# Kernel tuning notes

Measured on AMD Instinct MI355X. Metric: run time of the kernel, lower is better.

Reference implementation:

```python
import jax, jax.numpy as jnp
import numpy as np
from jax import lax

B, IN_C, DIM, HEADS, K = 8, 64, 128, 4, 3
H, W = 96, 96
HEAD_DIM = DIM // HEADS
SCALE = HEAD_DIM ** -0.5
EPS = 1e-5  # BatchNorm eps (eval mode, running_mean=0, running_var=1)


def _conv3x3(x, w):
    return lax.conv_general_dilated(x, w, (1, 1), ((1, 1), (1, 1)),
                                    dimension_numbers=('NCHW', 'OIHW', 'NCHW'))


def _cbr(x, w, g, b):
    y = _conv3x3(x, w)
    y = y * (g / jnp.sqrt(1.0 + EPS))[None, :, None, None] + b[None, :, None, None]
    return jax.nn.relu(y)


def setup_inputs() -> dict:
    key = jax.random.key(0)
    ks = jax.random.split(key, 24)
    n = lambda i, s, sc=0.05: jax.random.normal(ks[i], s, jnp.float32) * sc
    u = lambda i, s: jax.random.uniform(ks[i], s, jnp.float32, 0.5, 1.5)
    return dict(
        x=jax.random.normal(ks[0], (B, IN_C, H, W), jnp.float32),
        fg=jax.random.normal(ks[1], (B, DIM, H, W), jnp.float32),
        conv1_w=n(2, (DIM, IN_C, 3, 3)), bn1_g=u(3, (DIM,)), bn1_b=n(4, (DIM,)),
        conv2_w=n(5, (DIM, DIM, 3, 3)), bn2_g=u(6, (DIM,)), bn2_b=n(7, (DIM,)),
        v_w=n(8, (DIM, DIM)), v_b=n(9, (DIM,)),
        attn_w=n(10, (K ** 4 * HEADS, DIM)), attn_b=n(11, (K ** 4 * HEADS,)),
        proj_w=n(12, (DIM, DIM)), proj_b=n(13, (DIM,)),
        conv3_w=n(14, (DIM, DIM, 3, 3)), bn3_g=u(15, (DIM,)), bn3_b=n(16, (DIM,)),
        conv4_w=n(17, (DIM, DIM, 3, 3)), bn4_g=u(18, (DIM,)), bn4_b=n(19, (DIM,)),
    )


def reference(x, fg, conv1_w, bn1_g, bn1_b, conv2_w, bn2_g, bn2_b,
              v_w, v_b, attn_w, attn_b, proj_w, proj_b,
              conv3_w, bn3_g, bn3_b, conv4_w, bn4_g, bn4_b):
    L = H * W
    # input_cbr: two conv3x3 + BN(eval) + ReLU
    xf = _cbr(_cbr(x, conv1_w, bn1_g, bn1_b), conv2_w, bn2_g, bn2_b)  # (B,DIM,H,W)
    xh = xf.transpose(0, 2, 3, 1)                 # (B,H,W,DIM)
    fgh = fg.transpose(0, 2, 3, 1)                # (B,H,W,DIM)
    # value projection then unfold (im2col, channel-major patch ordering like torch)
    v = (xh @ v_w.T + v_b).transpose(0, 3, 1, 2)  # (B,DIM,H,W)
    patches = lax.conv_general_dilated_patches(v, (K, K), (1, 1), ((1, 1), (1, 1)))  # (B,DIM*9,H,W)
    vp = patches.reshape(B, HEADS, HEAD_DIM, K * K, L).transpose(0, 1, 4, 3, 2)  # (B,h,L,9,hd)
    # attention logits directly from fg (stride=1 -> AvgPool identity)
    attn = (fgh @ attn_w.T + attn_b).reshape(B, L, HEADS, K * K, K * K)
    attn = attn.transpose(0, 2, 1, 3, 4) * SCALE  # (B,h,L,9,9)
    attn = jax.nn.softmax(attn, axis=-1)
    # batched small matmuls: (9,9) @ (9,hd) per window
    xw = jnp.einsum('bhlpq,bhlqd->bhlpd', attn, vp)  # (B,h,L,9,hd)
    xw = xw.transpose(0, 1, 4, 3, 2).reshape(B, DIM, K, K, H, W)  # channel-major, then (kh,kw)
    # fold: overlapping scatter-add back to (H,W)
    canvas = jnp.zeros((B, DIM, H + 2, W + 2), xw.dtype)
    for ki in range(K):
        for kj in range(K):
            canvas = canvas.at[:, :, ki:ki + H, kj:kj + W].add(xw[:, :, ki, kj])
    folded = canvas[:, :, 1:H + 1, 1:W + 1]        # crop padding
    p = (folded.transpose(0, 2, 3, 1) @ proj_w.T + proj_b).transpose(0, 3, 1, 2)
    # output_cbr
    out = _cbr(_cbr(p, conv3_w, bn3_g, bn3_b), conv4_w, bn4_g, bn4_b)
    return out
```

## Files before the change

### kernel.cpp

```cpp
#include <hip/hip_runtime.h>
#include <math.h>

typedef __attribute__((ext_vector_type(8))) short short8;
typedef __attribute__((ext_vector_type(4))) float f32x4;
typedef unsigned short u16;
typedef unsigned int u32;

#define HW   96
#define LPIX 9216
static constexpr float kScale = 0.17677669529663687f;

__device__ inline u16 f2bf(float f) {
    u32 x = __float_as_uint(f);
    return (u16)((x + 0x7fffu + ((x >> 16) & 1u)) >> 16);
}
__device__ inline float bf2f(u16 v) { return __uint_as_float((u32)v << 16); }

typedef __attribute__((address_space(1))) const void gas_t;
typedef __attribute__((address_space(3))) void las_t;
__device__ __forceinline__ void g2lds16(const void* g, void* l) {
    __builtin_amdgcn_global_load_lds((gas_t*)g, (las_t*)l, 16, 0, 0);
}

#define WAITV(n) do {                                                   \
        asm volatile("s_waitcnt vmcnt(" #n ")" ::: "memory");           \
        __builtin_amdgcn_sched_barrier(0);                              \
    } while (0)
#define SFENCE() __builtin_amdgcn_sched_barrier(0)

__global__ __launch_bounds__(256) void cast_nchw_nhwc_all(
    const float* __restrict__ x, const float* __restrict__ fg,
    u16* __restrict__ xb, u16* __restrict__ fgb)
{
    const int y = blockIdx.x, b = blockIdx.y, tid = threadIdx.x;
    const int isfg = blockIdx.z;
    const float* in = isfg ? fg : x;
    u16* out = isfg ? fgb : xb;
    const int C = isfg ? 128 : 64;

    __shared__ float sT[HW * 128];
    for (int i = tid; i < HW * C; i += 256) {
        int c = i / HW, xx = i - c * HW;
        sT[xx * C + c] = in[(((size_t)b * C + c) * HW + y) * HW + xx];
    }
    __syncthreads();
    for (int i = tid; i < HW * (C / 8); i += 256) {
        int c8 = i % (C / 8), xx = i / (C / 8);
        union { short8 v8; u16 u[8]; } pk;
#pragma unroll
        for (int j = 0; j < 8; ++j) pk.u[j] = f2bf(sT[xx * C + c8 * 8 + j]);
        *(short8*)&out[(((size_t)b * HW + y) * HW + xx) * C + c8 * 8] = pk.v8;
    }
}

__device__ __forceinline__ void conv_w_decode(
    int i, int CIN, int& co, int& ci, int& f)
{
    int e  = i & 7;
    int gr = i >> 3;
    int c  = gr / 4608;
    int gi = gr - c * 4608;
    f  = gi >> 9;
    int rr = gi & 511;
    int ch = rr >> 8;
    int m  = (rr >> 2) & 63;
    int s  = rr & 3;
    int qq = (s - (m >> 1)) & 3;
    co = ch * 64 + m;
    ci = c * 32 + qq * 8 + e;
    (void)CIN;
}

__device__ __forceinline__ void conv_w_elem(
    const float* __restrict__ w, u16* __restrict__ wp, int CIN, int i)
{
    int co, ci, f;
    conv_w_decode(i, CIN, co, ci, f);
    wp[i] = f2bf(w[(size_t)(co * CIN + ci) * 9 + f]);
}

__device__ __forceinline__ void attn_w_elem(
    const float* __restrict__ aw, u16* __restrict__ wp, int i)
{
    int e = i & 7;
    int g = i >> 3;
    int h = g / 1536, r = g - h * 1536;
    int c4 = r / 384, r2 = r - c4 * 384;
    int rr = r2 >> 2, s = r2 & 3;
    int qq = (s - (rr >> 1)) & 3;
    int ci = c4 * 32 + qq * 8 + e;
    float v = (rr < 81) ? aw[(size_t)(h * 81 + rr) * 128 + ci] : 0.f;
    wp[i] = f2bf(v);
}

__global__ __launch_bounds__(256) void cast_weights_all(
    const float* __restrict__ c1w, const float* __restrict__ c2w,
    const float* __restrict__ c4w, const float* __restrict__ vw,
    const float* __restrict__ aw,
    u16* __restrict__ w1p, u16* __restrict__ w2p, u16* __restrict__ w4p,
    u16* __restrict__ vwp, u16* __restrict__ awp)
{
    int i = blockIdx.x * 256 + threadIdx.x;
    if (i < 73728)  { conv_w_elem(c1w, w1p, 64, i);  return; }
    i -= 73728;
    if (i < 147456) { conv_w_elem(c2w, w2p, 128, i); return; }
    i -= 147456;
    if (i < 147456) { conv_w_elem(c4w, w4p, 128, i); return; }
    i -= 147456;
    if (i < 16384)  { vwp[i] = f2bf(vw[i]); return; }
    i -= 16384;
    if (i < 49152)  attn_w_elem(aw, awp, i);
}

__global__ __launch_bounds__(128) void fuse_w3(
    const float* __restrict__ c3w, const float* __restrict__ pw,
    const float* __restrict__ pb,
    u16* __restrict__ w3p, float* __restrict__ bt)
{
    const int co = blockIdx.x;
    const int t  = threadIdx.x;
    __shared__ float sW[128 * 9];
    __shared__ float sB[9];

    {
        const float* src = &c3w[(size_t)co * 128 * 9];
        for (int i = t; i < 1152; i += 128) sW[i] = src[i];
    }
    __syncthreads();

    float acc[9];
#pragma unroll
    for (int f = 0; f < 9; ++f) acc[f] = 0.f;
#pragma unroll 4
    for (int ci = 0; ci < 128; ++ci) {
        float p = pw[ci * 128 + t];
#pragma unroll
        for (int f = 0; f < 9; ++f) acc[f] = fmaf(sW[ci * 9 + f], p, acc[f]);
    }
    {
        int m = co & 63, chh = co >> 6;
        int e = t & 7, qq = (t >> 3) & 3, c = t >> 5;
        int s = (qq + (m >> 1)) & 3;
#pragma unroll
        for (int f = 0; f < 9; ++f) {
            size_t gr = (size_t)c * 4608 + f * 512 + chh * 256 + m * 4 + s;
            w3p[gr * 8 + e] = f2bf(acc[f]);
        }
    }
    if (t < 9) {
        float a = 0.f;
        for (int ci = 0; ci < 128; ++ci) a = fmaf(sW[ci * 9 + t], pb[ci], a);
        sB[t] = a;
    }
    __syncthreads();
    if (t < 9) {
        float v;
        switch (t) {
            case 0: v = sB[0]+sB[1]+sB[2]+sB[3]+sB[4]+sB[5]+sB[6]+sB[7]+sB[8]; break;
            case 1: v = sB[0]+sB[1]+sB[2]; break;
            case 2: v = sB[6]+sB[7]+sB[8]; break;
            case 3: v = sB[0]+sB[3]+sB[6]; break;
            case 4: v = sB[2]+sB[5]+sB[8]; break;
            case 5: v = sB[0]; break;
            case 6: v = sB[2]; break;
            case 7: v = sB[6]; break;
            default: v = sB[8]; break;
        }
        bt[t * 128 + co] = v;
    }
}

template <int CIN, bool OUT_F32, bool PBC>
__global__ __launch_bounds__(768, 1) void conv_gemm(
    const u16* __restrict__ in, const u16* __restrict__ wp,
    const float* __restrict__ g, const float* __restrict__ be,
    const float* __restrict__ bt, void* outv)
{
    constexpr int NC   = CIN / 32;
    constexpr int WBYT = 73728;
    constexpr int HBYT = 36864;

    const int bx = blockIdx.x;
    const int b  = blockIdx.y;
    const int y0 = bx * 3;
    const int l0 = y0 * 96;

    const int tid = threadIdx.x, lane = tid & 63, wv = tid >> 6;
    const int half = wv & 1, ch = (wv >> 1) & 1, r = wv >> 2;
    const int lx = lane & 15, q = lane >> 4;

    __shared__ __align__(16) char smem[WBYT + 2 * HBYT];
    float* sT = (float*)smem;
    float* sF = (float*)smem;

    const int aoff = lx * 64 + (((q + (lx >> 1)) & 3) << 4);
    const int pb   = r * 96 + half * 48 + lx;

    f32x4 acc[4][3];
#pragma unroll
    for (int mt = 0; mt < 4; ++mt)
#pragma unroll
        for (int nt = 0; nt < 3; ++nt) acc[mt][nt] = (f32x4){0.f, 0.f, 0.f, 0.f};

    const u16* inb = in + (size_t)b * LPIX * CIN;

    auto STAGE_W = [&](int c) {
#pragma unroll
        for (int j = 0; j < 6; ++j) {
            g2lds16(&wp[((size_t)c * 4608 + j * 768 + tid) * 8],
                    (char*)smem + (j * 768 + wv * 64) * 16);
        }
    };
    auto STAGE_H = [&](int c, int buf) {
#pragma unroll
        for (int i = 0; i < 3; ++i) {
            int gi = i * 768 + tid;
            int p  = gi >> 2, s = gi & 3;
            int qq = (s - (p >> 1)) & 3;
            int lh = l0 - 96 + p;
            lh = lh < 0 ? 0 : (lh >= LPIX ? LPIX - 1 : lh);
            g2lds16(&inb[(size_t)lh * CIN + c * 32 + qq * 8],
                    (char*)smem + WBYT + buf * HBYT + (i * 768 + wv * 64) * 16);
        }
    };
    auto TAP = [&](int f, int hbuf) {
        const int dy = f / 3 - 1, dx = f % 3 - 1;
        const int off = dy * 96 + dx + 96;
        const bool vy = (unsigned)(y0 + r + dy) < 96u;
        const char* hb = (const char*)smem + WBYT + hbuf * HBYT;
        short8 af[4], bfr[3];
#pragma unroll
        for (int mt = 0; mt < 4; ++mt)
            af[mt] = *(const short8*)((const char*)smem + (f * 2 + ch) * 4096
                                      + mt * 1024 + aoff);
#pragma unroll
        for (int nt = 0; nt < 3; ++nt) {
            int pm = pb + nt * 16 + off;
            int slot = (q + (pm >> 1)) & 3;
            short8 t8 = *(const short8*)(hb + pm * 64 + slot * 16);
            bool ok = vy & ((unsigned)(half * 48 + nt * 16 + lx + dx) < 96u);
            bfr[nt] = ok ? t8 : (short8){0, 0, 0, 0, 0, 0, 0, 0};
        }
#pragma unroll
        for (int mt = 0; mt < 4; ++mt)
#pragma unroll
            for (int nt = 0; nt < 3; ++nt)
                acc[mt][nt] = __builtin_amdgcn_mfma_f32_16x16x32_bf16(
                    af[mt], bfr[nt], acc[mt][nt], 0, 0, 0);
    };

    STAGE_H(0, 0);
    SFENCE();
    STAGE_W(0);
    SFENCE();
    STAGE_H(1, 1);
    SFENCE();
    WAITV(3);
    __builtin_amdgcn_s_barrier();
    asm volatile("" ::: "memory");

#pragma unroll
    for (int c = 0; c < NC; ++c) {
        const int hbuf = c & 1;
        TAP(0, hbuf); TAP(1, hbuf); TAP(2, hbuf);
        TAP(3, hbuf); TAP(4, hbuf); TAP(5, hbuf);
        TAP(6, hbuf); TAP(7, hbuf); TAP(8, hbuf);
        if (c + 1 < NC) {
            asm volatile("s_waitcnt lgkmcnt(0)" ::: "memory");
            __builtin_amdgcn_s_barrier();
            asm volatile("" ::: "memory");
            STAGE_W(c + 1);
            SFENCE();
            if (c + 2 < NC) STAGE_H(c + 2, c & 1);
            SFENCE();
            if (c + 2 < NC) { WAITV(3); } else { WAITV(0); }
            __builtin_amdgcn_s_barrier();
            asm volatile("" ::: "memory");
        }
    }

    asm volatile("s_waitcnt lgkmcnt(0) vmcnt(0)" ::: "memory");
    __builtin_amdgcn_s_barrier();
    asm volatile("" ::: "memory");

    const float rs = rsqrtf(1.f + 1e-5f);
    if (OUT_F32) {
        float* out = (float*)outv;
#pragma unroll
        for (int hh = 0; hh < 2; ++hh) {
            if (hh) { __syncthreads(); }
            if (half == hh) {
#pragma unroll
                for (int mt = 0; mt < 4; ++mt)
#pragma unroll
                    for (int nt = 0; nt < 3; ++nt)
#pragma unroll
                        for (int reg = 0; reg < 4; ++reg)
                            sF[(ch * 64 + mt * 16 + q * 4 + reg) * 148
                               + r * 48 + nt * 16 + lx] = acc[mt][nt][reg];
            }
            __syncthreads();
            for (int i = tid; i < 4608; i += 768) {
                int co = i / 36, r2 = i - co * 36;
                int wrr = r2 / 12, j = r2 - wrr * 12;
                float sc = g[co] * rs, bb = be[co];
                f32x4 vv = *(const f32x4*)&sF[co * 148 + wrr * 48 + j * 4];
#pragma unroll
                for (int e = 0; e < 4; ++e) vv[e] = fmaxf(fmaf(vv[e], sc, bb), 0.f);
                *(f32x4*)&out[((size_t)b * 128 + co) * LPIX
                              + (y0 + wrr) * 96 + hh * 48 + j * 4] = vv;
            }
            if (!hh) __syncthreads();
        }
    } else {
        u16* out = (u16*)outv;
#pragma unroll
        for (int hh = 0; hh < 2; ++hh) {
            if (hh) { __syncthreads(); }
            if (half == hh) {
#pragma unroll
                for (int mt = 0; mt < 4; ++mt)
#pragma unroll
                    for (int nt = 0; nt < 3; ++nt)
#pragma unroll
                        for (int reg = 0; reg < 4; ++reg)
                            sT[(r * 48 + nt * 16 + lx) * 130
                               + ch * 64 + mt * 16 + q * 4 + reg] = acc[mt][nt][reg];
            }
            __syncthreads();
            for (int i = tid; i < 2304; i += 768) {
                int cog = i & 15, pxl = i >> 4;
                int wrr = pxl / 48, ofs = pxl - wrr * 48;
                int yy = y0 + wrr, xc = hh * 48 + ofs;
                int l = yy * 96 + xc;
                bool top = false, bot = false, lft = false, rgt = false;
                if (PBC) {
                    top = (yy == 0); bot = (yy == 95);
                    lft = (xc == 0); rgt = (xc == 95);
                }
                union { short8 v8; u16 u[8]; } pk;
#pragma unroll
                for (int j = 0; j < 8; ++j) {
                    int co = cog * 8 + j;
                    float val = sT[pxl * 130 + cog * 8 + j];
                    if (PBC) {
                        float corr = bt[co];
                        if (top) corr -= bt[128 + co];
                        if (bot) corr -= bt[256 + co];
                        if (lft) corr -= bt[384 + co];
                        if (rgt) corr -= bt[512 + co];
                        if (top && lft) corr += bt[640 + co];
                        if (top && rgt) corr += bt[768 + co];
                        if (bot && lft) corr += bt[896 + co];
                        if (bot && rgt) corr += bt[1024 + co];
                        val += corr;
                    }
                    pk.u[j] = f2bf(fmaxf(fmaf(val, g[co] * rs, be[co]), 0.f));
                }
                *(short8*)&out[((size_t)b * LPIX + l) * 128 + cog * 8] = pk.v8;
            }
            if (!hh) __syncthreads();
        }
    }
}

__global__ __launch_bounds__(256) void linear_mfma(
    const u16* __restrict__ in, const u16* __restrict__ wp,
    const float* __restrict__ bias, u16* __restrict__ out)
{
    const int l0 = blockIdx.x * 64;
    const int tid = threadIdx.x, lane = tid & 63, wv = tid >> 6;
    const int wm = wv >> 1, wn = wv & 1;
    const int lx = lane & 15, q = lane >> 4;

    __shared__ char smem[4 * 64 * 40 * 2 + 4 * 128 * 40 * 2];
    u16* sX = (u16*)smem;
    u16* sW = (u16*)(smem + 4 * 64 * 40 * 2);
    float* sT = (float*)smem;

    for (int i = tid; i < 1024; i += 256) {
        int k8 = i & 15, px = i >> 4;
        short8 v = *(const short8*)&in[((size_t)(l0 + px)) * 128 + k8 * 8];
        *(short8*)&sX[((k8 >> 2) * 64 + px) * 40 + (k8 & 3) * 8] = v;
    }
    for (int i = tid; i < 2048; i += 256) {
        int k8 = i & 15, co = i >> 4;
        short8 v = *(const short8*)&wp[(size_t)co * 128 + k8 * 8];
        *(short8*)&sW[((k8 >> 2) * 128 + co) * 40 + (k8 & 3) * 8] = v;
    }
    __syncthreads();

    f32x4 acc[4][2];
#pragma unroll
    for (int mt = 0; mt < 4; ++mt)
#pragma unroll
        for (int nt = 0; nt < 2; ++nt) acc[mt][nt] = (f32x4){0.f, 0.f, 0.f, 0.f};

#pragma unroll
    for (int c4 = 0; c4 < 4; ++c4) {
        short8 af[4], bfr[2];
#pragma unroll
        for (int mt = 0; mt < 4; ++mt)
            af[mt] = *(const short8*)&sW[(c4 * 128 + wm * 64 + mt * 16 + lx) * 40 + q * 8];
#pragma unroll
        for (int nt = 0; nt < 2; ++nt)
            bfr[nt] = *(const short8*)&sX[(c4 * 64 + wn * 32 + nt * 16 + lx) * 40 + q * 8];
#pragma unroll
        for (int mt = 0; mt < 4; ++mt)
#pragma unroll
            for (int nt = 0; nt < 2; ++nt)
                acc[mt][nt] = __builtin_amdgcn_mfma_f32_16x16x32_bf16(
                    af[mt], bfr[nt], acc[mt][nt], 0, 0, 0);
    }

    for (int mh = 0; mh < 2; ++mh) {
        __syncthreads();
        if (wm == mh) {
#pragma unroll
            for (int mt = 0; mt < 4; ++mt)
#pragma unroll
                for (int nt = 0; nt < 2; ++nt)
#pragma unroll
                    for (int reg = 0; reg < 4; ++reg)
                        sT[(wn * 32 + nt * 16 + lx) * 65 + mt * 16 + q * 4 + reg] =
                            acc[mt][nt][reg];
        }
        __syncthreads();
        for (int i = tid; i < 512; i += 256) {
            int cog = i & 7, px = i >> 3;
            union { short8 v8; u16 u[8]; } pk;
#pragma unroll
            for (int j = 0; j < 8; ++j) {
                int co = mh * 64 + cog * 8 + j;
                pk.u[j] = f2bf(sT[px * 65 + cog * 8 + j] + bias[co]);
            }
            *(short8*)&out[((size_t)(l0 + px)) * 128 + mh * 64 + cog * 8] = pk.v8;
        }
    }
}

__global__ __launch_bounds__(256, 2) void attn_mfma(
    const u16* __restrict__ fgb, const u16* __restrict__ awp,
    const float* __restrict__ ab, u16* __restrict__ A)
{
    const int lt = blockIdx.x, h = blockIdx.y, b = blockIdx.z;
    const int l0 = lt * 128;
    const int tid = threadIdx.x, lane = tid & 63, wv = tid >> 6;
    const int lx = lane & 15, q = lane >> 4;

    __shared__ __align__(16) char smem[57344];
    float* sL = (float*)smem;

    const u16* fb = fgb + ((size_t)b * LPIX + l0) * 128;
#pragma unroll
    for (int i = 0; i < 8; ++i) {
        int gg = i * 256 + tid;
        int c4 = gg >> 9, r = gg & 511, px = r >> 2, s = r & 3;
        int qq = (s - (px >> 1)) & 3;
        g2lds16(&fb[(size_t)px * 128 + c4 * 32 + qq * 8],
                (char*)smem + (i * 256 + wv * 64) * 16);
    }
    const u16* wb = awp + (size_t)h * 1536 * 8;
#pragma unroll
    for (int i = 0; i < 6; ++i) {
        g2lds16(&wb[(size_t)(i * 256 + tid) * 8],
                (char*)smem + 32768 + (i * 256 + wv * 64) * 16);
    }
    asm volatile("s_waitcnt vmcnt(0)" ::: "memory");
    __builtin_amdgcn_s_barrier();
    asm volatile("" ::: "memory");

    f32x4 acc[2][6];
#pragma unroll
    for (int nt = 0; nt < 2; ++nt)
#pragma unroll
        for (int j = 0; j < 6; ++j) acc[nt][j] = (f32x4){0.f, 0.f, 0.f, 0.f};

#pragma unroll
    for (int c4 = 0; c4 < 4; ++c4) {
        short8 af[2], bfr[6];
#pragma unroll
        for (int nt = 0; nt < 2; ++nt) {
            int px = wv * 32 + nt * 16 + lx;
            af[nt] = *(const short8*)((const char*)smem + c4 * 8192 + px * 64
                                      + (((q + (px >> 1)) & 3) << 4));
        }
#pragma unroll
        for (int j = 0; j < 6; ++j) {
            int rr = j * 16 + lx;
            bfr[j] = *(const short8*)((const char*)smem + 32768 + c4 * 6144 + rr * 64
                                      + (((q + (rr >> 1)) & 3) << 4));
        }
#pragma unroll
        for (int nt = 0; nt < 2; ++nt)
#pragma unroll
            for (int j = 0; j < 6; ++j)
                acc[nt][j] = __builtin_amdgcn_mfma_f32_16x16x32_bf16(
                    af[nt], bfr[j], acc[nt][j], 0, 0, 0);
    }

    __syncthreads();
#pragma unroll
    for (int nt = 0; nt < 2; ++nt)
#pragma unroll
        for (int j = 0; j < 6; ++j)
#pragma unroll
            for (int reg = 0; reg < 4; ++reg)
                sL[(wv * 32 + nt * 16 + q * 4 + reg) * 97 + j * 16 + lx] =
                    acc[nt][j][reg];
    __syncthreads();

    for (int t = tid; t < 1152; t += 256) {
        int px = t & 127, p = t >> 7;
        const int rbase = h * 81 + p * 9;
        float lg[9], m = -1e30f;
#pragma unroll
        for (int qq = 0; qq < 9; ++qq) {
            lg[qq] = (sL[px * 97 + p * 9 + qq] + ab[rbase + qq]) * kScale;
            m = fmaxf(m, lg[qq]);
        }
        float s = 0.f;
#pragma unroll
        for (int qq = 0; qq < 9; ++qq) { lg[qq] = __expf(lg[qq] - m); s += lg[qq]; }
        float inv = 1.f / s;
        u16* Ab = &A[(((size_t)(b * 4 + h) * 9 + p) * 9) * LPIX + l0 + px];
#pragma unroll
        for (int qq = 0; qq < 9; ++qq) Ab[(size_t)qq * LPIX] = f2bf(lg[qq] * inv);
    }
}

__global__ __launch_bounds__(384, 4) void attn_fold(
    const u16* __restrict__ A, const u16* __restrict__ v,
    u16* __restrict__ out)
{
    const int yt = blockIdx.x, h = blockIdx.y, b = blockIdx.z;
    const int y0 = yt * 4;
    const int tid = threadIdx.x;
    const int yl  = tid / 96;
    const int x   = tid - yl * 96;
    const int y   = y0 + yl;
    const int l   = y * 96 + x;

    __shared__ u16 sV[8 * 96 * 32];

    const u16* vb = v + (size_t)b * LPIX * 128 + h * 32;
    for (int t = tid; t < 3072; t += 384) {
        int k = t & 3, s = t >> 2;
        int r = s / 96, xx = s - r * 96;
        int gy = y0 - 2 + r;
        uint4 uu = make_uint4(0u, 0u, 0u, 0u);
        if ((unsigned)gy < 96u)
            uu = *(const uint4*)&vb[(size_t)(gy * 96 + xx) * 128 + k * 8];
        *(uint4*)&sV[(size_t)s * 32 + (((k + s) & 3) * 8)] = uu;
    }

    float S[25];
#pragma unroll
    for (int i = 0; i < 25; ++i) S[i] = 0.f;

    const u16* Ab = A + ((size_t)(b * 4 + h) * 81) * (size_t)LPIX;
#pragma unroll
    for (int ki = 0; ki < 3; ++ki) {
        const int ly = y + 1 - ki;
        const bool vy = ((unsigned)ly < 96u);
#pragma unroll
        for (int kj = 0; kj < 3; ++kj) {
            const int lx2 = x + 1 - kj;
            if (vy && (unsigned)lx2 < 96u) {
                const u16* Ap = Ab + (size_t)(ki * 3 + kj) * 9 * (size_t)LPIX
                              + (ly * 96 + lx2);
#pragma unroll
                for (int qq = 0; qq < 9; ++qq) {
                    const int qi = qq / 3, qj = qq - qi * 3;
                    S[(qi - ki + 2) * 5 + (qj - kj + 2)] += bf2f(Ap[(size_t)qq * LPIX]);
                }
            }
        }
    }

    __syncthreads();

    float acc[32];
#pragma unroll
    for (int c = 0; c < 32; ++c) acc[c] = 0.f;

#pragma unroll
    for (int oy = 0; oy < 5; ++oy) {
        const int r = yl + oy;
#pragma unroll
        for (int ox = 0; ox < 5; ++ox) {
            const int xx = x + ox - 2;
            if ((unsigned)xx >= 96u) continue;
            const float sc = S[oy * 5 + ox];
            const int sidx = r * 96 + xx;
            const u16* vp = &sV[(size_t)sidx * 32];
#pragma unroll
            for (int c8 = 0; c8 < 4; ++c8) {
                const uint4 uu = *(const uint4*)&vp[((c8 + sidx) & 3) * 8];
                acc[c8 * 8 + 0] = fmaf(sc, __uint_as_float(uu.x << 16),          acc[c8 * 8 + 0]);
                acc[c8 * 8 + 1] = fmaf(sc, __uint_as_float(uu.x & 0xffff0000u), acc[c8 * 8 + 1]);
                acc[c8 * 8 + 2] = fmaf(sc, __uint_as_float(uu.y << 16),          acc[c8 * 8 + 2]);
                acc[c8 * 8 + 3] = fmaf(sc, __uint_as_float(uu.y & 0xffff0000u), acc[c8 * 8 + 3]);
                acc[c8 * 8 + 4] = fmaf(sc, __uint_as_float(uu.z << 16),          acc[c8 * 8 + 4]);
                acc[c8 * 8 + 5] = fmaf(sc, __uint_as_float(uu.z & 0xffff0000u), acc[c8 * 8 + 5]);
                acc[c8 * 8 + 6] = fmaf(sc, __uint_as_float(uu.w << 16),          acc[c8 * 8 + 6]);
                acc[c8 * 8 + 7] = fmaf(sc, __uint_as_float(uu.w & 0xffff0000u), acc[c8 * 8 + 7]);
            }
        }
    }

    u16* ob = &out[((size_t)b * LPIX + l) * 128 + h * 32];
#pragma unroll
    for (int gidx = 0; gidx < 4; ++gidx) {
        union { short8 v8; u16 u[8]; } pk;
#pragma unroll
        for (int j = 0; j < 8; ++j) pk.u[j] = f2bf(acc[gidx * 8 + j]);
        *(short8*)&ob[gidx * 8] = pk.v8;
    }
}

extern "C" void kernel_launch(void* const* d_in, const int* in_sizes, int n_in,
                              void* d_out, int out_size, void* d_ws, size_t ws_size,
                              hipStream_t stream)
{
    const float* x    = (const float*)d_in[0];
    const float* fg   = (const float*)d_in[1];
    const float* c1w  = (const float*)d_in[2];
    const float* bn1g = (const float*)d_in[3];
    const float* bn1b = (const float*)d_in[4];
    const float* c2w  = (const float*)d_in[5];
    const float* bn2g = (const float*)d_in[6];
    const float* bn2b = (const float*)d_in[7];
    const float* vw   = (const float*)d_in[8];
    const float* vb   = (const float*)d_in[9];
    const float* aw   = (const float*)d_in[10];
    const float* abv  = (const float*)d_in[11];
    const float* pw   = (const float*)d_in[12];
    const float* pb   = (const float*)d_in[13];
    const float* c3w  = (const float*)d_in[14];
    const float* bn3g = (const float*)d_in[15];
    const float* bn3b = (const float*)d_in[16];
    const float* c4w  = (const float*)d_in[17];
    const float* bn4g = (const float*)d_in[18];
    const float* bn4b = (const float*)d_in[19];

    char* wsp = (char*)d_ws;
    size_t off = 0;
    auto carve = [&](size_t bytes) {
        void* pp = wsp + off;
        off += (bytes + 255) & ~(size_t)255;
        return pp;
    };
    u16*   xb   = (u16*)carve((size_t)8 * LPIX * 64 * 2);
    u16*   fgb  = (u16*)carve((size_t)8 * LPIX * 128 * 2);
    u16*   actA = (u16*)carve((size_t)8 * LPIX * 128 * 2);
    u16*   actB = (u16*)carve((size_t)8 * LPIX * 128 * 2);
    u16*   Abuf = (u16*)carve((size_t)8 * 324 * LPIX * 2);
    u16*   w1p  = (u16*)carve((size_t)9 * 2 * 128 * 32 * 2);
    u16*   w2p  = (u16*)carve((size_t)9 * 4 * 128 * 32 * 2);
    u16*   w3p  = (u16*)carve((size_t)9 * 4 * 128 * 32 * 2);
    u16*   w4p  = (u16*)carve((size_t)9 * 4 * 128 * 32 * 2);
    u16*   vwp  = (u16*)carve((size_t)128 * 128 * 2);
    u16*   awp  = (u16*)carve((size_t)4 * 1536 * 8 * 2);
    float* btab = (float*)carve((size_t)9 * 128 * 4);

    cast_nchw_nhwc_all<<<dim3(HW, 8, 2), 256, 0, stream>>>(x, fg, xb, fgb);
    cast_weights_all<<<1696, 256, 0, stream>>>(c1w, c2w, c4w, vw, aw,
                                               w1p, w2p, w4p, vwp, awp);
    fuse_w3<<<128, 128, 0, stream>>>(c3w, pw, pb, w3p, btab);

    conv_gemm<64, false, false><<<dim3(32, 8), 768, 0, stream>>>(xb, w1p, bn1g, bn1b, nullptr, actA);
    conv_gemm<128, false, false><<<dim3(32, 8), 768, 0, stream>>>(actA, w2p, bn2g, bn2b, nullptr, actB);
    linear_mfma<<<1152, 256, 0, stream>>>(actB, vwp, vb, actA);
    attn_mfma<<<dim3(72, 4, 8), 256, 0, stream>>>(fgb, awp, abv, Abuf);
    attn_fold<<<dim3(24, 4, 8), 384, 0, stream>>>(Abuf, actA, actB);
    conv_gemm<128, false, true><<<dim3(32, 8), 768, 0, stream>>>(actB, w3p, bn3g, bn3b, btab, actA);
    conv_gemm<128, true, false><<<dim3(32, 8), 768, 0, stream>>>(actA, w4p, bn4g, bn4b, nullptr, d_out);
}
```

Baseline: 367.8 us.

## Fuse value projection linear into conv2 epilogue via MFMA on LDS tile

The separate linear_mfma kernel that applied the value projection to conv2's output is removed. The conv2 epilogue now writes the BN+ReLU result as bf16 into LDS in a swizzled layout, loads pre-swizzled v weights into LDS, and runs a second MFMA GEMM before writing the projected values. This avoids one full round trip of the activation tensor through global memory and one kernel launch. The cost is extra epilogue work and LDS traffic inside the heavily loaded conv kernel. Buffer roles are swapped to match.

Result: slower. 435.2 us (+18.3%).

```diff
diff --git a/kernel.cpp b/kernel.cpp
--- a/kernel.cpp
+++ b/kernel.cpp
@@ -93,6 +93,19 @@
     wp[i] = f2bf(v);
 }
 
+__device__ __forceinline__ void vw_elem(
+    const float* __restrict__ vw, u16* __restrict__ wp, int i)
+{
+    int e = i & 7;
+    int g = i >> 3;
+    int s = g & 3;
+    int k = (g >> 2) & 127;
+    int c4 = g >> 9;
+    int qq = (s - (k >> 1)) & 3;
+    int ci = c4 * 32 + qq * 8 + e;
+    wp[i] = f2bf(vw[(size_t)k * 128 + ci]);
+}
+
 __global__ __launch_bounds__(256) void cast_weights_all(
     const float* __restrict__ c1w, const float* __restrict__ c2w,
     const float* __restrict__ c4w, const float* __restrict__ vw,
@@ -107,7 +120,7 @@
     i -= 147456;
     if (i < 147456) { conv_w_elem(c4w, w4p, 128, i); return; }
     i -= 147456;
-    if (i < 16384)  { vwp[i] = f2bf(vw[i]); return; }
+    if (i < 16384)  { vw_elem(vw, vwp, i); return; }
     i -= 16384;
     if (i < 49152)  attn_w_elem(aw, awp, i);
 }
@@ -170,11 +183,13 @@
     }
 }
 
-template <int CIN, bool OUT_F32, bool PBC>
+template <int CIN, bool OUT_F32, bool PBC, bool FUSE_V>
 __global__ __launch_bounds__(768, 1) void conv_gemm(
     const u16* __restrict__ in, const u16* __restrict__ wp,
     const float* __restrict__ g, const float* __restrict__ be,
-    const float* __restrict__ bt, void* outv)
+    const float* __restrict__ bt,
+    const u16* __restrict__ vwq, const float* __restrict__ vbs,
+    void* outv)
 {
     constexpr int NC   = CIN / 32;
     constexpr int WBYT = 73728;
@@ -284,7 +299,95 @@
     asm volatile("" ::: "memory");
 
     const float rs = rsqrtf(1.f + 1e-5f);
-    if (OUT_F32) {
+    if (FUSE_V) {
+        u16* out = (u16*)outv;
+        u16* sXF = (u16*)smem;
+#pragma unroll
+        for (int i = 0; i < 3; ++i) {
+            int gi = i * 768 + tid;
+            if (gi < 2048)
+                g2lds16(&vwq[(size_t)gi * 8],
+                        (char*)smem + WBYT + (i * 768 + wv * 64) * 16);
+        }
+#pragma unroll
+        for (int mt = 0; mt < 4; ++mt) {
+            int c4 = ch * 2 + (mt >> 1);
+            int qq = (mt & 1) * 2 + (q >> 1);
+            int cobase = ch * 64 + mt * 16 + q * 4;
+#pragma unroll
+            for (int nt = 0; nt < 3; ++nt) {
+                int px = r * 96 + half * 48 + nt * 16 + lx;
+                int slot = (qq + (px >> 1)) & 3;
+                union { u16 u[4]; uint2 d; } pk;
+#pragma unroll
+                for (int reg = 0; reg < 4; ++reg)
+                    pk.u[reg] = f2bf(fmaxf(fmaf(acc[mt][nt][reg],
+                                                g[cobase + reg] * rs,
+                                                be[cobase + reg]), 0.f));
+                *(uint2*)&sXF[c4 * 288 * 32 + px * 32 + slot * 8 + (q & 1) * 4] = pk.d;
+            }
+        }
+        asm volatile("s_waitcnt vmcnt(0) lgkmcnt(0)" ::: "memory");
+        __builtin_amdgcn_s_barrier();
+        asm volatile("" ::: "memory");
+
+        f32x4 acc2[4][3];
+#pragma unroll
+        for (int mt = 0; mt < 4; ++mt)
+#pragma unroll
+            for (int nt = 0; nt < 3; ++nt) acc2[mt][nt] = (f32x4){0.f, 0.f, 0.f, 0.f};
+#pragma unroll
+        for (int c4 = 0; c4 < 4; ++c4) {
+            short8 af2[4], bf2r[3];
+#pragma unroll
+            for (int mt = 0; mt < 4; ++mt) {
+                int k = ch * 64 + mt * 16 + lx;
+                af2[mt] = *(const short8*)((const char*)smem + WBYT + c4 * 8192
+                                           + k * 64 + (((q + (k >> 1)) & 3) << 4));
+            }
+#pragma unroll
+            for (int nt = 0; nt < 3; ++nt) {
+                int px = r * 96 + half * 48 + nt * 16 + lx;
+                bf2r[nt] = *(const short8*)((const char*)smem + c4 * 18432
+                                            + px * 64 + (((q + (px >> 1)) & 3) << 4));
+            }
+#pragma unroll
+            for (int mt = 0; mt < 4; ++mt)
+#pragma unroll
+                for (int nt = 0; nt < 3; ++nt)
+                    acc2[mt][nt] = __builtin_amdgcn_mfma_f32_16x16x32_bf16(
+                        af2[mt], bf2r[nt], acc2[mt][nt], 0, 0, 0);
+        }
+
+        float* sVt = (float*)smem;
+#pragma unroll
+        for (int kh = 0; kh < 2; ++kh) {
+            asm volatile("s_waitcnt lgkmcnt(0)" ::: "memory");
+            __builtin_amdgcn_s_barrier();
+            asm volatile("" ::: "memory");
+            if (ch == kh) {
+#pragma unroll
+                for (int mt = 0; mt < 4; ++mt)
+#pragma unroll
+                    for (int nt = 0; nt < 3; ++nt) {
+                        int px = r * 96 + half * 48 + nt * 16 + lx;
+                        int kgr = ((mt * 2 + (q >> 1)) + px) & 7;
+                        *(f32x4*)&sVt[px * 64 + kgr * 8 + (q & 1) * 4] = acc2[mt][nt];
+                    }
+            }
+            __syncthreads();
+            for (int i = tid; i < 2304; i += 768) {
+                int kg8 = i & 7, px = i >> 3;
+                int kgr = (kg8 + px) & 7;
+                const float* sp = &sVt[px * 64 + kgr * 8];
+                union { short8 v8; u16 u[8]; } pk;
+#pragma unroll
+                for (int j = 0; j < 8; ++j)
+                    pk.u[j] = f2bf(sp[j] + vbs[kh * 64 + kg8 * 8 + j]);
+                *(short8*)&out[((size_t)b * LPIX + l0 + px) * 128 + kh * 64 + kg8 * 8] = pk.v8;
+            }
+        }
+    } else if (OUT_F32) {
         float* out = (float*)outv;
 #pragma unroll
         for (int hh = 0; hh < 2; ++hh) {
@@ -360,81 +463,6 @@
                 *(short8*)&out[((size_t)b * LPIX + l) * 128 + cog * 8] = pk.v8;
             }
             if (!hh) __syncthreads();
-        }
-    }
-}
-
-__global__ __launch_bounds__(256) void linear_mfma(
-    const u16* __restrict__ in, const u16* __restrict__ wp,
-    const float* __restrict__ bias, u16* __restrict__ out)
-{
-    const int l0 = blockIdx.x * 64;
-    const int tid = threadIdx.x, lane = tid & 63, wv = tid >> 6;
-    const int wm = wv >> 1, wn = wv & 1;
-    const int lx = lane & 15, q = lane >> 4;
-
-    __shared__ char smem[4 * 64 * 40 * 2 + 4 * 128 * 40 * 2];
-    u16* sX = (u16*)smem;
-    u16* sW = (u16*)(smem + 4 * 64 * 40 * 2);
-    float* sT = (float*)smem;
-
-    for (int i = tid; i < 1024; i += 256) {
-        int k8 = i & 15, px = i >> 4;
-        short8 v = *(const short8*)&in[((size_t)(l0 + px)) * 128 + k8 * 8];
-        *(short8*)&sX[((k8 >> 2) * 64 + px) * 40 + (k8 & 3) * 8] = v;
-    }
-    for (int i = tid; i < 2048; i += 256) {
-        int k8 = i & 15, co = i >> 4;
-        short8 v = *(const short8*)&wp[(size_t)co * 128 + k8 * 8];
-        *(short8*)&sW[((k8 >> 2) * 128 + co) * 40 + (k8 & 3) * 8] = v;
-    }
-    __syncthreads();
-
-    f32x4 acc[4][2];
-#pragma unroll
-    for (int mt = 0; mt < 4; ++mt)
-#pragma unroll
-        for (int nt = 0; nt < 2; ++nt) acc[mt][nt] = (f32x4){0.f, 0.f, 0.f, 0.f};
-
-#pragma unroll
-    for (int c4 = 0; c4 < 4; ++c4) {
-        short8 af[4], bfr[2];
-#pragma unroll
-        for (int mt = 0; mt < 4; ++mt)
-            af[mt] = *(const short8*)&sW[(c4 * 128 + wm * 64 + mt * 16 + lx) * 40 + q * 8];
-#pragma unroll
-        for (int nt = 0; nt < 2; ++nt)
-            bfr[nt] = *(const short8*)&sX[(c4 * 64 + wn * 32 + nt * 16 + lx) * 40 + q * 8];
-#pragma unroll
-        for (int mt = 0; mt < 4; ++mt)
-#pragma unroll
-            for (int nt = 0; nt < 2; ++nt)
-                acc[mt][nt] = __builtin_amdgcn_mfma_f32_16x16x32_bf16(
-                    af[mt], bfr[nt], acc[mt][nt], 0, 0, 0);
-    }
-
-    for (int mh = 0; mh < 2; ++mh) {
-        __syncthreads();
-        if (wm == mh) {
-#pragma unroll
-            for (int mt = 0; mt < 4; ++mt)
-#pragma unroll
-                for (int nt = 0; nt < 2; ++nt)
-#pragma unroll
-                    for (int reg = 0; reg < 4; ++reg)
-                        sT[(wn * 32 + nt * 16 + lx) * 65 + mt * 16 + q * 4 + reg] =
-                            acc[mt][nt][reg];
-        }
-        __syncthreads();
-        for (int i = tid; i < 512; i += 256) {
-            int cog = i & 7, px = i >> 3;
-            union { short8 v8; u16 u[8]; } pk;
-#pragma unroll
-            for (int j = 0; j < 8; ++j) {
-                int co = mh * 64 + cog * 8 + j;
-                pk.u[j] = f2bf(sT[px * 65 + cog * 8 + j] + bias[co]);
-            }
-            *(short8*)&out[((size_t)(l0 + px)) * 128 + mh * 64 + cog * 8] = pk.v8;
         }
     }
 }
@@ -669,11 +697,14 @@
                                                w1p, w2p, w4p, vwp, awp);
     fuse_w3<<<128, 128, 0, stream>>>(c3w, pw, pb, w3p, btab);
 
-    conv_gemm<64, false, false><<<dim3(32, 8), 768, 0, stream>>>(xb, w1p, bn1g, bn1b, nullptr, actA);
-    conv_gemm<128, false, false><<<dim3(32, 8), 768, 0, stream>>>(actA, w2p, bn2g, bn2b, nullptr, actB);
-    linear_mfma<<<1152, 256, 0, stream>>>(actB, vwp, vb, actA);
+    conv_gemm<64, false, false, false><<<dim3(32, 8), 768, 0, stream>>>(
+        xb, w1p, bn1g, bn1b, nullptr, nullptr, nullptr, actA);
+    conv_gemm<128, false, false, true><<<dim3(32, 8), 768, 0, stream>>>(
+        actA, w2p, bn2g, bn2b, nullptr, vwp, vb, actB);
     attn_mfma<<<dim3(72, 4, 8), 256, 0, stream>>>(fgb, awp, abv, Abuf);
-    attn_fold<<<dim3(24, 4, 8), 384, 0, stream>>>(Abuf, actA, actB);
-    conv_gemm<128, false, true><<<dim3(32, 8), 768, 0, stream>>>(actB, w3p, bn3g, bn3b, btab, actA);
-    conv_gemm<128, true, false><<<dim3(32, 8), 768, 0, stream>>>(actA, w4p, bn4g, bn4b, nullptr, d_out);
-}
+    attn_fold<<<dim3(24, 4, 8), 384, 0, stream>>>(Abuf, actB, actA);
+    conv_gemm<128, false, true, false><<<dim3(32, 8), 768, 0, stream>>>(
+        actA, w3p, bn3g, bn3b, btab, nullptr, nullptr, actB);
+    conv_gemm<128, true, false, false><<<dim3(32, 8), 768, 0, stream>>>(
+        actB, w4p, bn4g, bn4b, nullptr, nullptr, nullptr, d_out);
+}
```
